# Performance work log

Measured on AMD Instinct MI355X. Metric: run time of the kernel, lower is better.

Reference implementation:

```python
import jax, jax.numpy as jnp
import numpy as np
import math

B, L, D = 2, 4096, 1024
K = D // 4


def _rotor(angles):
    # angles: [..., 6] -> scalar part s: [...], bivector part: [..., 6]
    mag = jnp.maximum(jnp.linalg.norm(angles, axis=-1), 1e-8)
    s = jnp.cos(mag)
    biv = (jnp.sin(mag) / mag)[..., None] * angles
    return s, biv


def _apply_rotor(s, biv, v):
    # s: [...], biv: [..., 6] (e12,e13,e14,e23,e24,e34), v: [..., 4]
    t12, t13, t14, t23, t24, t34 = (biv[..., i] for i in range(6))
    v1, v2, v3, v4 = (v[..., i] for i in range(4))
    s2 = s * s
    ts = 2.0 * s
    v1n = v1 * (s2 - t12 * t12 - t13 * t13 - t14 * t14) + ts * (v2 * t12 + v3 * t13 + v4 * t14)
    v2n = v2 * (s2 - t12 * t12 - t23 * t23 - t24 * t24) + ts * (-v1 * t12 + v3 * t23 + v4 * t24)
    v3n = v3 * (s2 - t13 * t13 - t23 * t23 - t34 * t34) + ts * (-v1 * t13 - v2 * t23 + v4 * t34)
    v4n = v4 * (s2 - t14 * t14 - t24 * t24 - t34 * t34) + ts * (-v1 * t14 - v2 * t24 - v3 * t34)
    return jnp.stack([v1n, v2n, v3n, v4n], axis=-1)


def _forward(x, wk1, bk1, wk2, bk2, wq1, bq1, wq2, bq2, wv, bv, ln_g, ln_b, wo, bo):
    b, l, d = x.shape
    k = d // 4
    gelu = lambda t: jax.nn.gelu(t, approximate=False)  # torch nn.GELU default = exact
    half_pi = math.pi / 2
    key_angles = (jnp.tanh(gelu(x @ wk1 + bk1) @ wk2 + bk2) * half_pi).reshape(b, l, k, 6)
    query_angles = (jnp.tanh(gelu(x @ wq1 + bq1) @ wq2 + bq2) * half_pi).reshape(b, l, k, 6)
    value = (x @ wv + bv).reshape(b, l, k, 4)
    ks, kb = _rotor(key_angles)
    qs, qb = _rotor(query_angles)
    rotated_value = _apply_rotor(ks, kb, value)          # [B,L,K,4]
    memory = jnp.cumsum(rotated_value, axis=1)            # running sum over sequence
    retrieved = _apply_rotor(qs, -qb, memory)             # reversed query rotor
    retrieved = retrieved.reshape(b, l, d)
    norm = jnp.sqrt(jnp.arange(1, l + 1, dtype=x.dtype))[None, :, None]
    r = retrieved / norm
    # LayerNorm (eps=1e-5) then Linear
    mu = jnp.mean(r, axis=-1, keepdims=True)
    var = jnp.mean((r - mu) ** 2, axis=-1, keepdims=True)
    rn = (r - mu) / jnp.sqrt(var + 1e-5) * ln_g + ln_b
    return x + rn @ wo + bo


def setup_inputs() -> dict:
    key = jax.random.key(0)
    ks = jax.random.split(key, 8)
    lin = lambda k, fi, fo: (jax.random.normal(k, (fi, fo), jnp.float32) * 0.02)
    return {
        "x": jax.random.normal(ks[0], (B, L, D), jnp.float32),
        "wk1": lin(ks[1], D, D), "bk1": jnp.zeros((D,), jnp.float32),
        "wk2": lin(ks[2], D, K * 6), "bk2": jnp.zeros((K * 6,), jnp.float32),
        "wq1": lin(ks[3], D, D), "bq1": jnp.zeros((D,), jnp.float32),
        "wq2": lin(ks[4], D, K * 6), "bq2": jnp.zeros((K * 6,), jnp.float32),
        "wv": lin(ks[5], D, D), "bv": jnp.zeros((D,), jnp.float32),
        "ln_g": jnp.ones((D,), jnp.float32), "ln_b": jnp.zeros((D,), jnp.float32),
        "wo": lin(ks[6], D, D), "bo": jnp.zeros((D,), jnp.float32),
    }


def reference(x, wk1, bk1, wk2, bk2, wq1, bq1, wq2, bq2, wv, bv, ln_g, ln_b, wo, bo):
    return _forward(x, wk1, bk1, wk2, bk2, wq1, bq1, wq2, bq2, wv, bv, ln_g, ln_b, wo, bo)
```

## Files before the change

kernel.cpp:

```cpp
#include <hip/hip_runtime.h>
#include <hip/hip_bf16.h>
#include <math.h>

#define D_DIM 1024
#define L_DIM 4096
#define B_DIM 2
#define K_DIM 256
#define N6    1536
#define M_ROWS 8192
#define CHUNKS 256
#define CHUNK_LEN 16
#define HALF_PI 1.57079632679489662f

typedef __attribute__((ext_vector_type(8))) short short8;
typedef __attribute__((ext_vector_type(4))) float f32x4;
typedef unsigned short us;

__device__ __forceinline__ void gload_lds16(const void* g, void* l) {
    __builtin_amdgcn_global_load_lds(
        (const __attribute__((address_space(1))) unsigned int*)g,
        (__attribute__((address_space(3))) unsigned int*)l,
        16, 0, 0);
}
__device__ __forceinline__ float bf2f(us u) {
    union { unsigned int i; float f; } c; c.i = ((unsigned int)u) << 16; return c.f;
}
__device__ __forceinline__ us f2bf(float v) {
    __hip_bfloat16 h = __float2bfloat16(v);
    return *(us*)&h;
}
__device__ __forceinline__ float tanh_fast(float x) {
    return 1.0f - 2.0f / (1.0f + __expf(2.0f * x));
}
__device__ __forceinline__ float gelu_exact(float v) {
    return 0.5f * v * (1.0f + erff(v * 0.70710678118654752f));
}

__device__ __forceinline__ void rotor_from_angles(const float a[6], float& s, float b[6]) {
    float m2 = a[0]*a[0] + a[1]*a[1] + a[2]*a[2] + a[3]*a[3] + a[4]*a[4] + a[5]*a[5];
    float mag = fmaxf(sqrtf(m2), 1e-8f);
    s = __cosf(mag);
    float f = __sinf(mag) / mag;
    #pragma unroll
    for (int i = 0; i < 6; ++i) b[i] = f * a[i];
}
__device__ __forceinline__ void apply_rotor(float s, const float b[6], const float v[4], float o[4]) {
    float t12 = b[0], t13 = b[1], t14 = b[2], t23 = b[3], t24 = b[4], t34 = b[5];
    float v1 = v[0], v2 = v[1], v3 = v[2], v4 = v[3];
    float s2 = s * s;
    float ts = 2.0f * s;
    o[0] = v1 * (s2 - t12*t12 - t13*t13 - t14*t14) + ts * ( v2*t12 + v3*t13 + v4*t14);
    o[1] = v2 * (s2 - t12*t12 - t23*t23 - t24*t24) + ts * (-v1*t12 + v3*t23 + v4*t24);
    o[2] = v3 * (s2 - t13*t13 - t23*t23 - t34*t34) + ts * (-v1*t13 - v2*t23 + v4*t34);
    o[3] = v4 * (s2 - t14*t14 - t24*t24 - t34*t34) + ts * (-v1*t14 - v2*t24 - v3*t34);
}

__global__ __launch_bounds__(256)
void transpose_cvt_kernel(const float* __restrict__ W, us* __restrict__ Wt, int Kd, int N)
{
    __shared__ float sh[32][33];
    int n0 = blockIdx.x * 32, k0 = blockIdx.y * 32;
    int tx = threadIdx.x & 31, ty = threadIdx.x >> 5;
    #pragma unroll
    for (int i = 0; i < 32; i += 8)
        sh[ty + i][tx] = W[(size_t)(k0 + ty + i) * N + n0 + tx];
    __syncthreads();
    #pragma unroll
    for (int i = 0; i < 32; i += 8)
        Wt[(size_t)(n0 + ty + i) * Kd + k0 + tx] = f2bf(sh[tx][ty + i]);
}

__global__ __launch_bounds__(256)
void cvt_bf16_kernel(const float* __restrict__ in, us* __restrict__ out)
{
    size_t i = ((size_t)blockIdx.x * 256 + threadIdx.x) * 8;
    float4 v0 = *(const float4*)(in + i);
    float4 v1 = *(const float4*)(in + i + 4);
    union { us u[8]; uint4 v; } pk;
    pk.u[0] = f2bf(v0.x); pk.u[1] = f2bf(v0.y); pk.u[2] = f2bf(v0.z); pk.u[3] = f2bf(v0.w);
    pk.u[4] = f2bf(v1.x); pk.u[5] = f2bf(v1.y); pk.u[6] = f2bf(v1.z); pk.u[7] = f2bf(v1.w);
    *(uint4*)(out + i) = pk.v;
}

__device__ __forceinline__ void gemm_core(
    const us* __restrict__ A, const us* __restrict__ Bt, int Kd,
    int bm, int bn, short* As, short* Bs, f32x4 acc[4][4])
{
    const int tid = threadIdx.x;
    const int l = tid & 63, w = tid >> 6;
    const int wr = w >> 1, wc = w & 1;
    const int srow = tid >> 2, schk = tid & 3;
    const int kch = schk ^ ((srow >> 1) & 3);
    const us* gA0 = A + (size_t)(bm + srow) * Kd + kch * 8;
    const us* gA1 = gA0 + (size_t)64 * Kd;
    const us* gB0 = Bt + (size_t)(bn + srow) * Kd + kch * 8;
    const us* gB1 = gB0 + (size_t)64 * Kd;
    short* dA0 = As + tid * 8;
    short* dA1 = As + 2048 + tid * 8;
    short* dB0 = Bs + tid * 8;
    short* dB1 = Bs + 2048 + tid * 8;

    const int fr = l & 15, fq = l >> 4;
    const int swz = fq ^ ((fr >> 1) & 3);
    const int aoff = (wr * 64 + fr) * 32 + swz * 8;
    const int boff = (wc * 64 + fr) * 32 + swz * 8;

    #pragma unroll
    for (int i = 0; i < 4; ++i)
        #pragma unroll
        for (int j = 0; j < 4; ++j)
            acc[i][j] = (f32x4){0.f, 0.f, 0.f, 0.f};

    const int nk = Kd >> 5;
    gload_lds16(gA0, dA0); gload_lds16(gA1, dA1);
    gload_lds16(gB0, dB0); gload_lds16(gB1, dB1);
    __syncthreads();
    int cur = 0;
    for (int t = 0; t < nk - 1; ++t) {
        const int k0 = (t + 1) * 32;
        const int nb = cur ^ 1;
        gload_lds16(gA0 + k0, dA0 + nb * 4096);
        gload_lds16(gA1 + k0, dA1 + nb * 4096);
        gload_lds16(gB0 + k0, dB0 + nb * 4096);
        gload_lds16(gB1 + k0, dB1 + nb * 4096);
        short8 af[4], bw[4];
        #pragma unroll
        for (int i = 0; i < 4; ++i) {
            af[i] = *(const short8*)&As[cur * 4096 + aoff + i * 512];
            bw[i] = *(const short8*)&Bs[cur * 4096 + boff + i * 512];
        }
        #pragma unroll
        for (int i = 0; i < 4; ++i)
            #pragma unroll
            for (int j = 0; j < 4; ++j)
                acc[i][j] = __builtin_amdgcn_mfma_f32_16x16x32_bf16(bw[j], af[i], acc[i][j], 0, 0, 0);
        __syncthreads();
        cur ^= 1;
    }
    {
        short8 af[4], bw[4];
        #pragma unroll
        for (int i = 0; i < 4; ++i) {
            af[i] = *(const short8*)&As[cur * 4096 + aoff + i * 512];
            bw[i] = *(const short8*)&Bs[cur * 4096 + boff + i * 512];
        }
        #pragma unroll
        for (int i = 0; i < 4; ++i)
            #pragma unroll
            for (int j = 0; j < 4; ++j)
                acc[i][j] = __builtin_amdgcn_mfma_f32_16x16x32_bf16(bw[j], af[i], acc[i][j], 0, 0, 0);
    }
}

__global__ __launch_bounds__(256)
void gemm_fused3(const us* __restrict__ xb,
                 const us* __restrict__ w0t, const us* __restrict__ w1t, const us* __restrict__ w2t,
                 const float* __restrict__ b0, const float* __restrict__ b1, const float* __restrict__ b2,
                 us* __restrict__ o0, us* __restrict__ o1, us* __restrict__ o2)
{
    __shared__ short As[2 * 4096];
    __shared__ short Bs[2 * 4096];
    const int bm = blockIdx.x * 128;
    const int r = blockIdx.y >> 3;
    const int bn = (blockIdx.y & 7) * 128;
    const us* Bt = (r == 0) ? w0t : (r == 1) ? w1t : w2t;
    const float* bias = (r == 0) ? b0 : (r == 1) ? b1 : b2;
    us* outp = (r == 0) ? o0 : (r == 1) ? o1 : o2;
    f32x4 acc[4][4];
    gemm_core(xb, Bt, D_DIM, bm, bn, As, Bs, acc);
    const int l = threadIdx.x & 63, w = threadIdx.x >> 6;
    const int wr = w >> 1, wc = w & 1, fr = l & 15, fq = l >> 4;
    #pragma unroll
    for (int i = 0; i < 4; ++i) {
        int row = bm + wr * 64 + i * 16 + fr;
        #pragma unroll
        for (int j = 0; j < 4; ++j) {
            int colb = bn + wc * 64 + j * 16 + fq * 4;
            float4 bs = *(const float4*)(bias + colb);
            float v0 = acc[i][j][0] + bs.x, v1 = acc[i][j][1] + bs.y;
            float v2 = acc[i][j][2] + bs.z, v3 = acc[i][j][3] + bs.w;
            if (r < 2) { v0 = gelu_exact(v0); v1 = gelu_exact(v1); v2 = gelu_exact(v2); v3 = gelu_exact(v3); }
            ushort4 pk; pk.x = f2bf(v0); pk.y = f2bf(v1); pk.z = f2bf(v2); pk.w = f2bf(v3);
            *(ushort4*)(outp + (size_t)row * D_DIM + colb) = pk;
        }
    }
}

__global__ __launch_bounds__(256)
void gemm_angles(const us* __restrict__ Hk, const us* __restrict__ Hq,
                 const us* __restrict__ wk2t, const us* __restrict__ wq2t,
                 const float* __restrict__ bk2, const float* __restrict__ bq2,
                 us* __restrict__ ak, us* __restrict__ aq)
{
    __shared__ short As[2 * 4096];
    __shared__ short Bs[2 * 4096];
    const int z = blockIdx.z;
    const us* A  = z ? Hq : Hk;
    const us* Bt = z ? wq2t : wk2t;
    const float* bias = z ? bq2 : bk2;
    us* outp = z ? aq : ak;
    const int bm = blockIdx.x * 128;
    const int bn = blockIdx.y * 128;
    f32x4 acc[4][4];
    gemm_core(A, Bt, D_DIM, bm, bn, As, Bs, acc);
    const int l = threadIdx.x & 63, w = threadIdx.x >> 6;
    const int wr = w >> 1, wc = w & 1, fr = l & 15, fq = l >> 4;
    #pragma unroll
    for (int i = 0; i < 4; ++i) {
        int row = bm + wr * 64 + i * 16 + fr;
        #pragma unroll
        for (int j = 0; j < 4; ++j) {
            int colb = bn + wc * 64 + j * 16 + fq * 4;
            float4 bs = *(const float4*)(bias + colb);
            ushort4 pk;
            pk.x = f2bf(tanh_fast(acc[i][j][0] + bs.x) * HALF_PI);
            pk.y = f2bf(tanh_fast(acc[i][j][1] + bs.y) * HALF_PI);
            pk.z = f2bf(tanh_fast(acc[i][j][2] + bs.z) * HALF_PI);
            pk.w = f2bf(tanh_fast(acc[i][j][3] + bs.w) * HALF_PI);
            *(ushort4*)(outp + (size_t)row * N6 + colb) = pk;
        }
    }
}

__global__ __launch_bounds__(256)
void gemm_final(const us* __restrict__ rn, const us* __restrict__ wot,
                const float* __restrict__ bo, const float* __restrict__ x,
                float* __restrict__ out)
{
    __shared__ short As[2 * 4096];
    __shared__ short Bs[2 * 4096];
    const int bm = blockIdx.x * 128;
    const int bn = blockIdx.y * 128;
    f32x4 acc[4][4];
    gemm_core(rn, wot, D_DIM, bm, bn, As, Bs, acc);
    const int l = threadIdx.x & 63, w = threadIdx.x >> 6;
    const int wr = w >> 1, wc = w & 1, fr = l & 15, fq = l >> 4;
    #pragma unroll
    for (int i = 0; i < 4; ++i) {
        int row = bm + wr * 64 + i * 16 + fr;
        #pragma unroll
        for (int j = 0; j < 4; ++j) {
            int colb = bn + wc * 64 + j * 16 + fq * 4;
            size_t off = (size_t)row * D_DIM + colb;
            float4 bs = *(const float4*)(bo + colb);
            float4 rx = *(const float4*)(x + off);
            float4 o;
            o.x = acc[i][j][0] + bs.x + rx.x;
            o.y = acc[i][j][1] + bs.y + rx.y;
            o.z = acc[i][j][2] + bs.z + rx.z;
            o.w = acc[i][j][3] + bs.w + rx.w;
            *(float4*)(out + off) = o;
        }
    }
}

__global__ __launch_bounds__(256)
void rot_chunk_sum(const us* __restrict__ value, const us* __restrict__ ak,
                   float4* __restrict__ sums)
{
    int bc = blockIdx.x;
    int b = bc >> 8, c = bc & 255;
    int k = threadIdx.x;
    float4 acc = make_float4(0.f, 0.f, 0.f, 0.f);
    size_t row0 = (size_t)b * L_DIM + c * CHUNK_LEN;
    for (int i = 0; i < CHUNK_LEN; ++i) {
        size_t row = row0 + i;
        ushort4 uv = *(const ushort4*)(value + row * D_DIM + k * 4);
        const unsigned int* ap = (const unsigned int*)(ak + row * N6 + k * 6);
        unsigned int a0 = ap[0], a1 = ap[1], a2 = ap[2];
        float a[6] = { bf2f(a0 & 0xffff), bf2f(a0 >> 16), bf2f(a1 & 0xffff),
                       bf2f(a1 >> 16), bf2f(a2 & 0xffff), bf2f(a2 >> 16) };
        float s, bb[6];
        rotor_from_angles(a, s, bb);
        float v[4] = {bf2f(uv.x), bf2f(uv.y), bf2f(uv.z), bf2f(uv.w)}, o[4];
        apply_rotor(s, bb, v, o);
        acc.x += o[0]; acc.y += o[1]; acc.z += o[2]; acc.w += o[3];
    }
    sums[(size_t)bc * 256 + k] = acc;
}

__global__ __launch_bounds__(256)
void scan_chunks_kernel(const float4* __restrict__ sums, float4* __restrict__ carry)
{
    int b = blockIdx.x >> 8;
    int k = blockIdx.x & 255;
    int c = threadIdx.x;
    __shared__ float4 sh[CHUNKS];
    float4 v = sums[((size_t)(b * CHUNKS + c)) * 256 + k];
    sh[c] = v;
    __syncthreads();
    for (int off = 1; off < CHUNKS; off <<= 1) {
        float4 t = make_float4(0.f, 0.f, 0.f, 0.f);
        if (c >= off) t = sh[c - off];
        __syncthreads();
        v.x += t.x; v.y += t.y; v.z += t.z; v.w += t.w;
        sh[c] = v;
        __syncthreads();
    }
    float4 ex = make_float4(0.f, 0.f, 0.f, 0.f);
    if (c > 0) ex = sh[c - 1];
    carry[((size_t)(b * CHUNKS + c)) * 256 + k] = ex;
}

__global__ __launch_bounds__(256)
void scan_apply_ln(const us* __restrict__ value, const us* __restrict__ ak,
                   const us* __restrict__ aq, const float4* __restrict__ carry,
                   const float* __restrict__ g, const float* __restrict__ bta,
                   us* __restrict__ rn)
{
    int bc = blockIdx.x;
    int b = bc >> 8, c = bc & 255;
    int k = threadIdx.x;
    int wv = k >> 6, lane = k & 63;
    float4 run = carry[(size_t)bc * 256 + k];
    float4 gv = *(const float4*)(g + k * 4);
    float4 bv = *(const float4*)(bta + k * 4);
    __shared__ float reds[4], redq[4];
    for (int i = 0; i < CHUNK_LEN; ++i) {
        int l = c * CHUNK_LEN + i;
        size_t row = (size_t)b * L_DIM + l;
        ushort4 uv = *(const ushort4*)(value + row * D_DIM + k * 4);
        const unsigned int* akp = (const unsigned int*)(ak + row * N6 + k * 6);
        unsigned int ka0 = akp[0], ka1 = akp[1], ka2 = akp[2];
        float a[6] = { bf2f(ka0 & 0xffff), bf2f(ka0 >> 16), bf2f(ka1 & 0xffff),
                       bf2f(ka1 >> 16), bf2f(ka2 & 0xffff), bf2f(ka2 >> 16) };
        float s, bb[6];
        rotor_from_angles(a, s, bb);
        float v[4] = {bf2f(uv.x), bf2f(uv.y), bf2f(uv.z), bf2f(uv.w)}, o[4];
        apply_rotor(s, bb, v, o);
        run.x += o[0]; run.y += o[1]; run.z += o[2]; run.w += o[3];
        const unsigned int* aqp = (const unsigned int*)(aq + row * N6 + k * 6);
        unsigned int qa0 = aqp[0], qa1 = aqp[1], qa2 = aqp[2];
        float aq6[6] = { bf2f(qa0 & 0xffff), bf2f(qa0 >> 16), bf2f(qa1 & 0xffff),
                         bf2f(qa1 >> 16), bf2f(qa2 & 0xffff), bf2f(qa2 >> 16) };
        float qs, qb[6];
        rotor_from_angles(aq6, qs, qb);
        #pragma unroll
        for (int t = 0; t < 6; ++t) qb[t] = -qb[t];
        float mem[4] = {run.x, run.y, run.z, run.w}, o2[4];
        apply_rotor(qs, qb, mem, o2);
        float inv = rsqrtf((float)(l + 1));
        o2[0] *= inv; o2[1] *= inv; o2[2] *= inv; o2[3] *= inv;
        float sm = o2[0] + o2[1] + o2[2] + o2[3];
        float qm = o2[0]*o2[0] + o2[1]*o2[1] + o2[2]*o2[2] + o2[3]*o2[3];
        #pragma unroll
        for (int off = 1; off < 64; off <<= 1) {
            sm += __shfl_xor(sm, off);
            qm += __shfl_xor(qm, off);
        }
        if (lane == 0) { reds[wv] = sm; redq[wv] = qm; }
        __syncthreads();
        sm = reds[0] + reds[1] + reds[2] + reds[3];
        qm = redq[0] + redq[1] + redq[2] + redq[3];
        float mu = sm * (1.0f / 1024.0f);
        float var = qm * (1.0f / 1024.0f) - mu * mu;
        float rstd = rsqrtf(var + 1e-5f);
        ushort4 pk;
        pk.x = f2bf((o2[0] - mu) * rstd * gv.x + bv.x);
        pk.y = f2bf((o2[1] - mu) * rstd * gv.y + bv.y);
        pk.z = f2bf((o2[2] - mu) * rstd * gv.z + bv.z);
        pk.w = f2bf((o2[3] - mu) * rstd * gv.w + bv.w);
        *(ushort4*)(rn + row * D_DIM + k * 4) = pk;
        __syncthreads();
    }
}

extern "C" void kernel_launch(void* const* d_in, const int* in_sizes, int n_in,
                              void* d_out, int out_size, void* d_ws, size_t ws_size,
                              hipStream_t stream)
{
    const float* x   = (const float*)d_in[0];
    const float* wk1 = (const float*)d_in[1];
    const float* bk1 = (const float*)d_in[2];
    const float* wk2 = (const float*)d_in[3];
    const float* bk2 = (const float*)d_in[4];
    const float* wq1 = (const float*)d_in[5];
    const float* bq1 = (const float*)d_in[6];
    const float* wq2 = (const float*)d_in[7];
    const float* bq2 = (const float*)d_in[8];
    const float* wv  = (const float*)d_in[9];
    const float* bv  = (const float*)d_in[10];
    const float* lng = (const float*)d_in[11];
    const float* lnb = (const float*)d_in[12];
    const float* wo  = (const float*)d_in[13];
    const float* bo  = (const float*)d_in[14];
    float* out = (float*)d_out;

    char* ws = (char*)d_ws;
    us* xb    = (us*)(ws);
    us* Hk    = (us*)(ws + (16ull  << 20));
    us* Hq    = (us*)(ws + (32ull  << 20));
    us* val   = (us*)(ws + (48ull  << 20));
    us* ak    = (us*)(ws + (64ull  << 20));
    us* aq    = (us*)(ws + (88ull  << 20));
    float4* sums  = (float4*)(ws + (112ull << 20));
    float4* carry = (float4*)(ws + (114ull << 20));
    us* wk1t  = (us*)(ws + (116ull << 20));
    us* wq1t  = (us*)(ws + (118ull << 20));
    us* wvt   = (us*)(ws + (120ull << 20));
    us* wot   = (us*)(ws + (122ull << 20));
    us* wk2t  = (us*)(ws + (124ull << 20));
    us* wq2t  = (us*)(ws + (127ull << 20));
    us* rn    = xb;

    dim3 blk(256);
    dim3 gt1(D_DIM / 32, D_DIM / 32);
    dim3 gt2(N6 / 32, D_DIM / 32);
    transpose_cvt_kernel<<<gt1, blk, 0, stream>>>(wk1, wk1t, D_DIM, D_DIM);
    transpose_cvt_kernel<<<gt1, blk, 0, stream>>>(wq1, wq1t, D_DIM, D_DIM);
    transpose_cvt_kernel<<<gt1, blk, 0, stream>>>(wv,  wvt,  D_DIM, D_DIM);
    transpose_cvt_kernel<<<gt1, blk, 0, stream>>>(wo,  wot,  D_DIM, D_DIM);
    transpose_cvt_kernel<<<gt2, blk, 0, stream>>>(wk2, wk2t, D_DIM, N6);
    transpose_cvt_kernel<<<gt2, blk, 0, stream>>>(wq2, wq2t, D_DIM, N6);
    cvt_bf16_kernel<<<dim3(M_ROWS * D_DIM / (256 * 8)), blk, 0, stream>>>(x, xb);

    gemm_fused3<<<dim3(M_ROWS / 128, 24), blk, 0, stream>>>(
        xb, wk1t, wq1t, wvt, bk1, bq1, bv, Hk, Hq, val);
    gemm_angles<<<dim3(M_ROWS / 128, N6 / 128, 2), blk, 0, stream>>>(
        Hk, Hq, wk2t, wq2t, bk2, bq2, ak, aq);
    rot_chunk_sum<<<dim3(B_DIM * CHUNKS), blk, 0, stream>>>(val, ak, sums);
    scan_chunks_kernel<<<dim3(B_DIM * K_DIM), blk, 0, stream>>>(sums, carry);
    scan_apply_ln<<<dim3(B_DIM * CHUNKS), blk, 0, stream>>>(val, ak, aq, carry, lng, lnb, rn);
    gemm_final<<<dim3(M_ROWS / 128, D_DIM / 128), blk, 0, stream>>>(rn, wot, bo, x, out);
}
```

Before: 270.0 us.

## Replace GEMM core with 256x256 tile, 8-wave ping-pong pipelined MFMA kernel

```diff
diff --git a/kernel.cpp b/kernel.cpp
--- a/kernel.cpp
+++ b/kernel.cpp
@@ -56,8 +56,14 @@
 }
 
 __global__ __launch_bounds__(256)
-void transpose_cvt_kernel(const float* __restrict__ W, us* __restrict__ Wt, int Kd, int N)
-{
+void transpose_cvt4(const float* __restrict__ w0, const float* __restrict__ w1,
+                    const float* __restrict__ w2, const float* __restrict__ w3,
+                    us* __restrict__ o0, us* __restrict__ o1,
+                    us* __restrict__ o2, us* __restrict__ o3, int Kd, int N)
+{
+    const float* W = (blockIdx.z == 0) ? w0 : (blockIdx.z == 1) ? w1 : (blockIdx.z == 2) ? w2 : w3;
+    us* Wt = (blockIdx.z == 0) ? o0 : (blockIdx.z == 1) ? o1 : (blockIdx.z == 2) ? o2 : o3;
+    if (W == nullptr) return;
     __shared__ float sh[32][33];
     int n0 = blockIdx.x * 32, k0 = blockIdx.y * 32;
     int tx = threadIdx.x & 31, ty = threadIdx.x >> 5;
@@ -82,173 +88,272 @@
     *(uint4*)(out + i) = pk.v;
 }
 
-__device__ __forceinline__ void gemm_core(
-    const us* __restrict__ A, const us* __restrict__ Bt, int Kd,
-    int bm, int bn, short* As, short* Bs, f32x4 acc[4][4])
+
+#define GBAR()  do { __builtin_amdgcn_s_barrier(); __builtin_amdgcn_sched_barrier(0); } while (0)
+
+__device__ __forceinline__ void stage_half32(const us* __restrict__ g, int Kd, int k0,
+                                             short* lh, int tid) {
+    int r = tid >> 2, ch = tid & 3;
+    int lch = ch ^ (r & 3);
+    gload_lds16(g + (size_t)r * Kd + k0 + lch * 8, lh + tid * 8);
+}
+
+__device__ __forceinline__ void gemm256_core(
+    const us* __restrict__ Ab, const us* __restrict__ Bb, int Kd,
+    short* lds, f32x4 (&acc)[8][4])
 {
     const int tid = threadIdx.x;
     const int l = tid & 63, w = tid >> 6;
-    const int wr = w >> 1, wc = w & 1;
-    const int srow = tid >> 2, schk = tid & 3;
-    const int kch = schk ^ ((srow >> 1) & 3);
-    const us* gA0 = A + (size_t)(bm + srow) * Kd + kch * 8;
-    const us* gA1 = gA0 + (size_t)64 * Kd;
-    const us* gB0 = Bt + (size_t)(bn + srow) * Kd + kch * 8;
-    const us* gB1 = gB0 + (size_t)64 * Kd;
-    short* dA0 = As + tid * 8;
-    short* dA1 = As + 2048 + tid * 8;
-    short* dB0 = Bs + tid * 8;
-    short* dB1 = Bs + 2048 + tid * 8;
-
+    const int wr = w >> 2, wc = w & 3;
     const int fr = l & 15, fq = l >> 4;
-    const int swz = fq ^ ((fr >> 1) & 3);
-    const int aoff = (wr * 64 + fr) * 32 + swz * 8;
-    const int boff = (wc * 64 + fr) * 32 + swz * 8;
-
-    #pragma unroll
-    for (int i = 0; i < 4; ++i)
+
+    #pragma unroll
+    for (int i = 0; i < 8; ++i)
         #pragma unroll
         for (int j = 0; j < 4; ++j)
             acc[i][j] = (f32x4){0.f, 0.f, 0.f, 0.f};
 
-    const int nk = Kd >> 5;
-    gload_lds16(gA0, dA0); gload_lds16(gA1, dA1);
-    gload_lds16(gB0, dB0); gload_lds16(gB1, dB1);
-    __syncthreads();
-    int cur = 0;
-    for (int t = 0; t < nk - 1; ++t) {
-        const int k0 = (t + 1) * 32;
-        const int nb = cur ^ 1;
-        gload_lds16(gA0 + k0, dA0 + nb * 4096);
-        gload_lds16(gA1 + k0, dA1 + nb * 4096);
-        gload_lds16(gB0 + k0, dB0 + nb * 4096);
-        gload_lds16(gB1 + k0, dB1 + nb * 4096);
-        short8 af[4], bw[4];
-        #pragma unroll
-        for (int i = 0; i < 4; ++i) {
-            af[i] = *(const short8*)&As[cur * 4096 + aoff + i * 512];
-            bw[i] = *(const short8*)&Bs[cur * 4096 + boff + i * 512];
-        }
-        #pragma unroll
-        for (int i = 0; i < 4; ++i)
-            #pragma unroll
-            for (int j = 0; j < 4; ++j)
-                acc[i][j] = __builtin_amdgcn_mfma_f32_16x16x32_bf16(bw[j], af[i], acc[i][j], 0, 0, 0);
-        __syncthreads();
-        cur ^= 1;
-    }
-    {
-        short8 af[4], bw[4];
-        #pragma unroll
-        for (int i = 0; i < 4; ++i) {
-            af[i] = *(const short8*)&As[cur * 4096 + aoff + i * 512];
-            bw[i] = *(const short8*)&Bs[cur * 4096 + boff + i * 512];
-        }
-        #pragma unroll
-        for (int i = 0; i < 4; ++i)
-            #pragma unroll
-            for (int j = 0; j < 4; ++j)
-                acc[i][j] = __builtin_amdgcn_mfma_f32_16x16x32_bf16(bw[j], af[i], acc[i][j], 0, 0, 0);
-    }
-}
-
-__global__ __launch_bounds__(256)
+    short* Ard = lds + wr * 4096;
+    short* Brd = lds + 8192 + (wc >> 1) * 4096;
+    const int brow = (wc & 1) * 64;
+    const int swch = (fq ^ (fr & 3)) * 8;
+
+    const int nkt = Kd >> 5;
+
+    stage_half32(Ab,            Kd, 0,  lds + 0,             tid);
+    stage_half32(Ab + 128*Kd,   Kd, 0,  lds + 4096,          tid);
+    stage_half32(Bb,            Kd, 0,  lds + 8192,          tid);
+    stage_half32(Bb + 128*Kd,   Kd, 0,  lds + 12288,         tid);
+    stage_half32(Bb,            Kd, 32, lds + 16384 + 8192,  tid);
+    stage_half32(Ab,            Kd, 32, lds + 16384,         tid);
+    asm volatile("s_waitcnt vmcnt(2)" ::: "memory");
+    GBAR();
+
+    short8 a0[4], a1[4], b0[2], b1[2];
+
+    for (int it = 0; it < (nkt >> 1); ++it) {
+        const int t1k = (2 * it + 1) * 32;
+        const int p0k = min(2 * it + 2, nkt - 1) * 32;
+        const int p1k = min(2 * it + 3, nkt - 1) * 32;
+
+        #pragma unroll
+        for (int mi = 0; mi < 4; ++mi)
+            a0[mi] = *(const short8*)(Ard + (mi * 16 + fr) * 32 + swch);
+        #pragma unroll
+        for (int ni = 0; ni < 2; ++ni)
+            b0[ni] = *(const short8*)(Brd + (brow + ni * 16 + fr) * 32 + swch);
+        stage_half32(Ab + 128*Kd, Kd, t1k, lds + 16384 + 4096, tid);
+        GBAR();
+        __builtin_amdgcn_s_setprio(1);
+        #pragma unroll
+        for (int mi = 0; mi < 4; ++mi)
+            #pragma unroll
+            for (int ni = 0; ni < 2; ++ni)
+                acc[mi][ni] = __builtin_amdgcn_mfma_f32_16x16x32_bf16(b0[ni], a0[mi], acc[mi][ni], 0, 0, 0);
+        __builtin_amdgcn_sched_barrier(0);
+        __builtin_amdgcn_s_setprio(0);
+        GBAR();
+
+        #pragma unroll
+        for (int ni = 0; ni < 2; ++ni)
+            b1[ni] = *(const short8*)(Brd + (brow + (ni + 2) * 16 + fr) * 32 + swch);
+        stage_half32(Bb + 128*Kd, Kd, t1k, lds + 16384 + 12288, tid);
+        GBAR();
+        __builtin_amdgcn_s_setprio(1);
+        #pragma unroll
+        for (int mi = 0; mi < 4; ++mi)
+            #pragma unroll
+            for (int ni = 0; ni < 2; ++ni)
+                acc[mi][ni + 2] = __builtin_amdgcn_mfma_f32_16x16x32_bf16(b1[ni], a0[mi], acc[mi][ni + 2], 0, 0, 0);
+        __builtin_amdgcn_sched_barrier(0);
+        __builtin_amdgcn_s_setprio(0);
+        GBAR();
+
+        #pragma unroll
+        for (int mi = 0; mi < 4; ++mi)
+            a1[mi] = *(const short8*)(Ard + ((mi + 4) * 16 + fr) * 32 + swch);
+        stage_half32(Bb, Kd, p0k, lds + 8192, tid);
+        GBAR();
+        __builtin_amdgcn_s_setprio(1);
+        #pragma unroll
+        for (int mi = 0; mi < 4; ++mi)
+            #pragma unroll
+            for (int ni = 0; ni < 2; ++ni)
+                acc[mi + 4][ni + 2] = __builtin_amdgcn_mfma_f32_16x16x32_bf16(b1[ni], a1[mi], acc[mi + 4][ni + 2], 0, 0, 0);
+        __builtin_amdgcn_sched_barrier(0);
+        __builtin_amdgcn_s_setprio(0);
+        GBAR();
+
+        stage_half32(Ab, Kd, p0k, lds + 0, tid);
+        GBAR();
+        __builtin_amdgcn_s_setprio(1);
+        #pragma unroll
+        for (int mi = 0; mi < 4; ++mi)
+            #pragma unroll
+            for (int ni = 0; ni < 2; ++ni)
+                acc[mi + 4][ni] = __builtin_amdgcn_mfma_f32_16x16x32_bf16(b0[ni], a1[mi], acc[mi + 4][ni], 0, 0, 0);
+        __builtin_amdgcn_sched_barrier(0);
+        __builtin_amdgcn_s_setprio(0);
+        asm volatile("s_waitcnt vmcnt(2)" ::: "memory");
+        GBAR();
+
+        #pragma unroll
+        for (int mi = 0; mi < 4; ++mi)
+            a0[mi] = *(const short8*)(Ard + 16384 + (mi * 16 + fr) * 32 + swch);
+        #pragma unroll
+        for (int ni = 0; ni < 2; ++ni)
+            b0[ni] = *(const short8*)(Brd + 16384 + (brow + ni * 16 + fr) * 32 + swch);
+        stage_half32(Ab + 128*Kd, Kd, p0k, lds + 4096, tid);
+        GBAR();
+        __builtin_amdgcn_s_setprio(1);
+        #pragma unroll
+        for (int mi = 0; mi < 4; ++mi)
+            #pragma unroll
+            for (int ni = 0; ni < 2; ++ni)
+                acc[mi][ni] = __builtin_amdgcn_mfma_f32_16x16x32_bf16(b0[ni], a0[mi], acc[mi][ni], 0, 0, 0);
+        __builtin_amdgcn_sched_barrier(0);
+        __builtin_amdgcn_s_setprio(0);
+        GBAR();
+
+        #pragma unroll
+        for (int ni = 0; ni < 2; ++ni)
+            b1[ni] = *(const short8*)(Brd + 16384 + (brow + (ni + 2) * 16 + fr) * 32 + swch);
+        stage_half32(Bb + 128*Kd, Kd, p0k, lds + 12288, tid);
+        GBAR();
+        __builtin_amdgcn_s_setprio(1);
+        #pragma unroll
+        for (int mi = 0; mi < 4; ++mi)
+            #pragma unroll
+            for (int ni = 0; ni < 2; ++ni)
+                acc[mi][ni + 2] = __builtin_amdgcn_mfma_f32_16x16x32_bf16(b1[ni], a0[mi], acc[mi][ni + 2], 0, 0, 0);
+        __builtin_amdgcn_sched_barrier(0);
+        __builtin_amdgcn_s_setprio(0);
+        GBAR();
+
+        #pragma unroll
+        for (int mi = 0; mi < 4; ++mi)
+            a1[mi] = *(const short8*)(Ard + 16384 + ((mi + 4) * 16 + fr) * 32 + swch);
+        stage_half32(Bb, Kd, p1k, lds + 16384 + 8192, tid);
+        GBAR();
+        __builtin_amdgcn_s_setprio(1);
+        #pragma unroll
+        for (int mi = 0; mi < 4; ++mi)
+            #pragma unroll
+            for (int ni = 0; ni < 2; ++ni)
+                acc[mi + 4][ni + 2] = __builtin_amdgcn_mfma_f32_16x16x32_bf16(b1[ni], a1[mi], acc[mi + 4][ni + 2], 0, 0, 0);
+        __builtin_amdgcn_sched_barrier(0);
+        __builtin_amdgcn_s_setprio(0);
+        GBAR();
+
+        stage_half32(Ab, Kd, p1k, lds + 16384, tid);
+        GBAR();
+        __builtin_amdgcn_s_setprio(1);
+        #pragma unroll
+        for (int mi = 0; mi < 4; ++mi)
+            #pragma unroll
+            for (int ni = 0; ni < 2; ++ni)
+                acc[mi + 4][ni] = __builtin_amdgcn_mfma_f32_16x16x32_bf16(b0[ni], a1[mi], acc[mi + 4][ni], 0, 0, 0);
+        __builtin_amdgcn_sched_barrier(0);
+        __builtin_amdgcn_s_setprio(0);
+        asm volatile("s_waitcnt vmcnt(2)" ::: "memory");
+        GBAR();
+    }
+}
+
+__global__ __launch_bounds__(512, 2)
 void gemm_fused3(const us* __restrict__ xb,
                  const us* __restrict__ w0t, const us* __restrict__ w1t, const us* __restrict__ w2t,
                  const float* __restrict__ b0, const float* __restrict__ b1, const float* __restrict__ b2,
                  us* __restrict__ o0, us* __restrict__ o1, us* __restrict__ o2)
 {
-    __shared__ short As[2 * 4096];
-    __shared__ short Bs[2 * 4096];
-    const int bm = blockIdx.x * 128;
-    const int r = blockIdx.y >> 3;
-    const int bn = (blockIdx.y & 7) * 128;
+    __shared__ short lds[32768];
+    const int bm = blockIdx.x * 256;
+    const int r = blockIdx.y >> 2;
+    const int bn = (blockIdx.y & 3) * 256;
     const us* Bt = (r == 0) ? w0t : (r == 1) ? w1t : w2t;
     const float* bias = (r == 0) ? b0 : (r == 1) ? b1 : b2;
     us* outp = (r == 0) ? o0 : (r == 1) ? o1 : o2;
-    f32x4 acc[4][4];
-    gemm_core(xb, Bt, D_DIM, bm, bn, As, Bs, acc);
+    f32x4 acc[8][4];
+    gemm256_core(xb + (size_t)bm * D_DIM, Bt + (size_t)bn * D_DIM, D_DIM, lds, acc);
     const int l = threadIdx.x & 63, w = threadIdx.x >> 6;
-    const int wr = w >> 1, wc = w & 1, fr = l & 15, fq = l >> 4;
-    #pragma unroll
-    for (int i = 0; i < 4; ++i) {
-        int row = bm + wr * 64 + i * 16 + fr;
-        #pragma unroll
-        for (int j = 0; j < 4; ++j) {
-            int colb = bn + wc * 64 + j * 16 + fq * 4;
-            float4 bs = *(const float4*)(bias + colb);
-            float v0 = acc[i][j][0] + bs.x, v1 = acc[i][j][1] + bs.y;
-            float v2 = acc[i][j][2] + bs.z, v3 = acc[i][j][3] + bs.w;
+    const int wr = w >> 2, wc = w & 3, fr = l & 15, fq = l >> 4;
+    #pragma unroll
+    for (int mi = 0; mi < 8; ++mi) {
+        int row = bm + wr * 128 + mi * 16 + fr;
+        #pragma unroll
+        for (int ni = 0; ni < 4; ++ni) {
+            int col = bn + wc * 64 + ni * 16 + fq * 4;
+            float4 bs = *(const float4*)(bias + col);
+            float v0 = acc[mi][ni][0] + bs.x, v1 = acc[mi][ni][1] + bs.y;
+            float v2 = acc[mi][ni][2] + bs.z, v3 = acc[mi][ni][3] + bs.w;
             if (r < 2) { v0 = gelu_exact(v0); v1 = gelu_exact(v1); v2 = gelu_exact(v2); v3 = gelu_exact(v3); }
             ushort4 pk; pk.x = f2bf(v0); pk.y = f2bf(v1); pk.z = f2bf(v2); pk.w = f2bf(v3);
-            *(ushort4*)(outp + (size_t)row * D_DIM + colb) = pk;
+            *(ushort4*)(outp + (size_t)row * D_DIM + col) = pk;
         }
     }
 }
 
-__global__ __launch_bounds__(256)
+__global__ __launch_bounds__(512, 2)
 void gemm_angles(const us* __restrict__ Hk, const us* __restrict__ Hq,
                  const us* __restrict__ wk2t, const us* __restrict__ wq2t,
                  const float* __restrict__ bk2, const float* __restrict__ bq2,
                  us* __restrict__ ak, us* __restrict__ aq)
 {
-    __shared__ short As[2 * 4096];
-    __shared__ short Bs[2 * 4096];
+    __shared__ short lds[32768];
     const int z = blockIdx.z;
     const us* A  = z ? Hq : Hk;
     const us* Bt = z ? wq2t : wk2t;
     const float* bias = z ? bq2 : bk2;
     us* outp = z ? aq : ak;
-    const int bm = blockIdx.x * 128;
-    const int bn = blockIdx.y * 128;
-    f32x4 acc[4][4];
-    gemm_core(A, Bt, D_DIM, bm, bn, As, Bs, acc);
+    const int bm = blockIdx.x * 256;
+    const int bn = blockIdx.y * 256;
+    f32x4 acc[8][4];
+    gemm256_core(A + (size_t)bm * D_DIM, Bt + (size_t)bn * D_DIM, D_DIM, lds, acc);
     const int l = threadIdx.x & 63, w = threadIdx.x >> 6;
-    const int wr = w >> 1, wc = w & 1, fr = l & 15, fq = l >> 4;
-    #pragma unroll
-    for (int i = 0; i < 4; ++i) {
-        int row = bm + wr * 64 + i * 16 + fr;
-        #pragma unroll
-        for (int j = 0; j < 4; ++j) {
-            int colb = bn + wc * 64 + j * 16 + fq * 4;
-            float4 bs = *(const float4*)(bias + colb);
+    const int wr = w >> 2, wc = w & 3, fr = l & 15, fq = l >> 4;
+    #pragma unroll
+    for (int mi = 0; mi < 8; ++mi) {
+        int row = bm + wr * 128 + mi * 16 + fr;
+        #pragma unroll
+        for (int ni = 0; ni < 4; ++ni) {
+            int col = bn + wc * 64 + ni * 16 + fq * 4;
+            float4 bs = *(const float4*)(bias + col);
             ushort4 pk;
-            pk.x = f2bf(tanh_fast(acc[i][j][0] + bs.x) * HALF_PI);
-            pk.y = f2bf(tanh_fast(acc[i][j][1] + bs.y) * HALF_PI);
-            pk.z = f2bf(tanh_fast(acc[i][j][2] + bs.z) * HALF_PI);
-            pk.w = f2bf(tanh_fast(acc[i][j][3] + bs.w) * HALF_PI);
-            *(ushort4*)(outp + (size_t)row * N6 + colb) = pk;
+            pk.x = f2bf(tanh_fast(acc[mi][ni][0] + bs.x) * HALF_PI);
+            pk.y = f2bf(tanh_fast(acc[mi][ni][1] + bs.y) * HALF_PI);
+            pk.z = f2bf(tanh_fast(acc[mi][ni][2] + bs.z) * HALF_PI);
+            pk.w = f2bf(tanh_fast(acc[mi][ni][3] + bs.w) * HALF_PI);
+            *(ushort4*)(outp + (size_t)row * N6 + col) = pk;
         }
     }
 }
 
-__global__ __launch_bounds__(256)
+__global__ __launch_bounds__(512, 2)
 void gemm_final(const us* __restrict__ rn, const us* __restrict__ wot,
                 const float* __restrict__ bo, const float* __restrict__ x,
                 float* __restrict__ out)
 {
-    __shared__ short As[2 * 4096];
-    __shared__ short Bs[2 * 4096];
-    const int bm = blockIdx.x * 128;
-    const int bn = blockIdx.y * 128;
-    f32x4 acc[4][4];
-    gemm_core(rn, wot, D_DIM, bm, bn, As, Bs, acc);
+    __shared__ short lds[32768];
+    const int bm = blockIdx.x * 256;
+    const int bn = blockIdx.y * 256;
+    f32x4 acc[8][4];
+    gemm256_core(rn + (size_t)bm * D_DIM, wot + (size_t)bn * D_DIM, D_DIM, lds, acc);
     const int l = threadIdx.x & 63, w = threadIdx.x >> 6;
-    const int wr = w >> 1, wc = w & 1, fr = l & 15, fq = l >> 4;
-    #pragma unroll
-    for (int i = 0; i < 4; ++i) {
-        int row = bm + wr * 64 + i * 16 + fr;
-        #pragma unroll
-        for (int j = 0; j < 4; ++j) {
-            int colb = bn + wc * 64 + j * 16 + fq * 4;
-            size_t off = (size_t)row * D_DIM + colb;
-            float4 bs = *(const float4*)(bo + colb);
+    const int wr = w >> 2, wc = w & 3, fr = l & 15, fq = l >> 4;
+    #pragma unroll
+    for (int mi = 0; mi < 8; ++mi) {
+        int row = bm + wr * 128 + mi * 16 + fr;
+        #pragma unroll
+        for (int ni = 0; ni < 4; ++ni) {
+            int col = bn + wc * 64 + ni * 16 + fq * 4;
+            size_t off = (size_t)row * D_DIM + col;
+            float4 bs = *(const float4*)(bo + col);
             float4 rx = *(const float4*)(x + off);
             float4 o;
-            o.x = acc[i][j][0] + bs.x + rx.x;
-            o.y = acc[i][j][1] + bs.y + rx.y;
-            o.z = acc[i][j][2] + bs.z + rx.z;
-            o.w = acc[i][j][3] + bs.w + rx.w;
+            o.x = acc[mi][ni][0] + bs.x + rx.x;
+            o.y = acc[mi][ni][1] + bs.y + rx.y;
+            o.z = acc[mi][ni][2] + bs.z + rx.z;
+            o.w = acc[mi][ni][3] + bs.w + rx.w;
             *(float4*)(out + off) = o;
         }
     }
@@ -404,22 +509,19 @@
     us* rn    = xb;
 
     dim3 blk(256);
-    dim3 gt1(D_DIM / 32, D_DIM / 32);
-    dim3 gt2(N6 / 32, D_DIM / 32);
-    transpose_cvt_kernel<<<gt1, blk, 0, stream>>>(wk1, wk1t, D_DIM, D_DIM);
-    transpose_cvt_kernel<<<gt1, blk, 0, stream>>>(wq1, wq1t, D_DIM, D_DIM);
-    transpose_cvt_kernel<<<gt1, blk, 0, stream>>>(wv,  wvt,  D_DIM, D_DIM);
-    transpose_cvt_kernel<<<gt1, blk, 0, stream>>>(wo,  wot,  D_DIM, D_DIM);
-    transpose_cvt_kernel<<<gt2, blk, 0, stream>>>(wk2, wk2t, D_DIM, N6);
-    transpose_cvt_kernel<<<gt2, blk, 0, stream>>>(wq2, wq2t, D_DIM, N6);
+    transpose_cvt4<<<dim3(D_DIM / 32, D_DIM / 32, 4), blk, 0, stream>>>(
+        wk1, wq1, wv, wo, wk1t, wq1t, wvt, wot, D_DIM, D_DIM);
+    transpose_cvt4<<<dim3(N6 / 32, D_DIM / 32, 2), blk, 0, stream>>>(
+        wk2, wq2, nullptr, nullptr, wk2t, wq2t, nullptr, nullptr, D_DIM, N6);
     cvt_bf16_kernel<<<dim3(M_ROWS * D_DIM / (256 * 8)), blk, 0, stream>>>(x, xb);
 
-    gemm_fused3<<<dim3(M_ROWS / 128, 24), blk, 0, stream>>>(
+    dim3 blk512(512);
+    gemm_fused3<<<dim3(M_ROWS / 256, 12), blk512, 0, stream>>>(
         xb, wk1t, wq1t, wvt, bk1, bq1, bv, Hk, Hq, val);
-    gemm_angles<<<dim3(M_ROWS / 128, N6 / 128, 2), blk, 0, stream>>>(
+    gemm_angles<<<dim3(M_ROWS / 256, N6 / 256, 2), blk512, 0, stream>>>(
         Hk, Hq, wk2t, wq2t, bk2, bq2, ak, aq);
     rot_chunk_sum<<<dim3(B_DIM * CHUNKS), blk, 0, stream>>>(val, ak, sums);
     scan_chunks_kernel<<<dim3(B_DIM * K_DIM), blk, 0, stream>>>(sums, carry);
     scan_apply_ln<<<dim3(B_DIM * CHUNKS), blk, 0, stream>>>(val, ak, aq, carry, lng, lnb, rn);
-    gemm_final<<<dim3(M_ROWS / 128, D_DIM / 128), blk, 0, stream>>>(rn, wot, bo, x, out);
-}
+    gemm_final<<<dim3(M_ROWS / 256, D_DIM / 256), blk512, 0, stream>>>(rn, wot, bo, x, out);
+}
```

New measurement: 293.9 us. 8.9% more time.
